# Optimization experiments

Measured on AMD Instinct MI355X. Metric: run time of the kernel, lower is better.

Reference implementation:

```python
import jax, jax.numpy as jnp
from jax import lax
import numpy as np

NUM_TAGS = 128
B, S = 256, 512


def setup_inputs() -> dict:
    key = jax.random.key(0)
    k1, k2, k3 = jax.random.split(key, 3)
    emissions = jax.random.normal(k1, (B, S, NUM_TAGS), dtype=jnp.float32)
    tags = jax.random.randint(k2, (B, S), 0, NUM_TAGS, dtype=jnp.int64)
    mask = jnp.ones((B, S), dtype=bool)
    transitions = jax.random.normal(k3, (NUM_TAGS, NUM_TAGS), dtype=jnp.float32)
    return {"emissions": emissions, "tags": tags, "mask": mask, "transitions": transitions}


def reference(emissions, tags, mask, transitions):
    # emissions: [B,S,C], tags: [B,S] int, mask: [B,S] bool, transitions: [C,C]
    m = mask.astype(emissions.dtype)

    # --- gold score (vectorized over time) ---
    emit = jnp.take_along_axis(emissions, tags[..., None], axis=2)[..., 0]  # [B,S]
    trans = transitions[tags[:, :-1], tags[:, 1:]]                           # [B,S-1]
    gold = jnp.sum(emit * m) + jnp.sum(trans * m[:, 1:])

    # --- partition via forward algorithm (note: original masks cancel out:
    # alpha*mask + alpha*~mask == alpha, so partition ignores mask) ---
    def step(alpha, e_t):
        # alpha: [B,C] prev log-alpha, e_t: [B,C] emissions at t
        score = alpha[:, :, None] + transitions[None, :, :] + e_t[:, None, :]  # [B,C,C]
        return jax.nn.logsumexp(score, axis=1), None

    alpha0 = emissions[:, 0]                       # [B,C]
    em_rest = jnp.swapaxes(emissions[:, 1:], 0, 1) # [S-1,B,C]
    alpha, _ = lax.scan(step, alpha0, em_rest)
    partition = jnp.sum(jax.nn.logsumexp(alpha, axis=1))

    # forward returns -log_likelihood = partition - gold
    return partition - gold
```

## Files before the change

### kernel.cpp

```cpp
#include <hip/hip_runtime.h>

#define NT 128
#define SS 512
#define PW 132

typedef float f32x2 __attribute__((ext_vector_type(2)));

__device__ __forceinline__ float rdlane(float v, int lane) {
    return __int_as_float(__builtin_amdgcn_readlane(__float_as_int(v), lane));
}
__device__ __forceinline__ int fexp_of(float x) {
    return (int)((__float_as_uint(x) >> 23) & 0xFFu) - 127;
}
__device__ __forceinline__ void lds_barrier() {
    asm volatile("s_waitcnt lgkmcnt(0)\n\ts_barrier" ::: "memory");
}

__global__ void zero_out_kernel(float* out) { out[0] = 0.0f; }

__global__ __launch_bounds__(256, 1) void crf_fwd_kernel(
    const float* __restrict__ emissions,
    const int* __restrict__ tags,
    const unsigned char* __restrict__ mask,
    const float* __restrict__ trans,
    float* __restrict__ out)
{
    const int b   = blockIdx.x;
    const int tid = threadIdx.x;
    const int l   = tid & 63;
    const int w   = tid >> 6;
    const int st  = (w << 5) + (l & 31);

    __shared__ float pbuf[2][4 * PW];
    __shared__ int   kbuf[4];
    __shared__ float redf[4];
    __shared__ float redg[4];

    const float*         emB = emissions + (size_t)b * SS * NT;
    const int*           tgB = tags + b * SS;
    const unsigned char* mkB = mask + b * SS;

    float gold = 0.0f;
    for (int t = tid; t < SS; t += 256) {
        int tg   = tgB[t];
        float mk = mkB[t] ? 1.0f : 0.0f;
        float a  = emB[(size_t)t * NT + tg];
        if (t > 0) a += trans[tgB[t - 1] * NT + tg];
        gold += a * mk;
    }

    f32x2 eTr[32];
    #pragma unroll
    for (int r = 0; r < 32; r++) {
        const float* row = trans + (size_t)((w << 5) + r) * NT;
        f32x2 v; v.x = __expf(row[l]); v.y = __expf(row[l + 64]);
        eTr[r] = v;
    }

    float a0 = emB[st];
    {
        float v = a0;
        #pragma unroll
        for (int o = 16; o > 0; o >>= 1) v = fmaxf(v, __shfl_xor(v, o));
        if (l == 0) redf[w] = v;
    }
    __syncthreads();
    const float M0 = fmaxf(fmaxf(redf[0], redf[1]), fmaxf(redf[2], redf[3]));

    float p = __expf(a0 - M0);
    float S = 0.0f;
    int K = 0, kv_own = 0;

    float ex_o = __expf(emB[(size_t)1 * NT + st]);
    float ex_e = __expf(emB[(size_t)2 * NT + st]);
    float pd_o = emB[(size_t)3 * NT + st];
    float pd_e = emB[(size_t)4 * NT + st];

    auto matvec = [&](int q, bool kw) -> float {
        f32x2 A0 = {0.f,0.f}, A1 = {0.f,0.f}, A2 = {0.f,0.f}, A3 = {0.f,0.f};
        #pragma unroll
        for (int r = 0; r < 32; r += 4) {
            float q0 = rdlane(p, r + 0);
            float q1 = rdlane(p, r + 1);
            float q2 = rdlane(p, r + 2);
            float q3 = rdlane(p, r + 3);
            f32x2 b0 = {q0, q0}, b1 = {q1, q1}, b2 = {q2, q2}, b3 = {q3, q3};
            A0 = __builtin_elementwise_fma(b0, eTr[r + 0], A0);
            A1 = __builtin_elementwise_fma(b1, eTr[r + 1], A1);
            A2 = __builtin_elementwise_fma(b2, eTr[r + 2], A2);
            A3 = __builtin_elementwise_fma(b3, eTr[r + 3], A3);
        }
        f32x2 s2 = (A0 + A1) + (A2 + A3);
        pbuf[q][w * PW + l]      = s2.x;
        pbuf[q][w * PW + l + 64] = s2.y;
        if (kw && l == 0) kbuf[w] = kv_own;
        lds_barrier();
        return (pbuf[q][0 * PW + st] + pbuf[q][1 * PW + st]) +
               (pbuf[q][2 * PW + st] + pbuf[q][3 * PW + st]);
    };
    auto rot = [&](int t, float& pd, float& ex) {
        float nr = pd;
        int tn = t + 4; if (tn > SS - 1) tn = SS - 1;
        pd = emB[(size_t)tn * NT + st];
        ex = __expf(nr);
    };

    #pragma unroll 1
    for (int t = 1; t < SS; t += 4) {
        {
            float sn = matvec(1, false) * ex_o;
            p = ldexpf(sn, -K);
            S += (float)K;
            int kv = fexp_of(p);
            #pragma unroll
            for (int o = 16; o > 0; o >>= 1) kv = max(kv, __shfl_xor(kv, o));
            kv_own = kv;
            rot(t, pd_o, ex_o);
        }
        if (t + 1 < SS) {
            float sn = matvec(0, true) * ex_e;
            int k0 = kbuf[0], k1 = kbuf[1], k2 = kbuf[2], k3 = kbuf[3];
            K = max(max(k0, k1), max(k2, k3));
            p = sn;
            rot(t + 1, pd_e, ex_e);
        }
        if (t + 2 < SS) { p = matvec(1, false) * ex_o; rot(t + 2, pd_o, ex_o); }
        if (t + 3 < SS) { p = matvec(0, false) * ex_e; rot(t + 3, pd_e, ex_e); }
    }

    {
        float sw = (l < 32) ? p : 0.0f;
        float g  = gold;
        #pragma unroll
        for (int o = 32; o > 0; o >>= 1) {
            sw += __shfl_xor(sw, o);
            g  += __shfl_xor(g, o);
        }
        if (l == 0) { redf[w] = sw; redg[w] = g; }
    }
    __syncthreads();
    if (tid == 0) {
        float tot  = (redf[0] + redf[1]) + (redf[2] + redf[3]);
        float part = M0 + S * 0.69314718055994531f + __logf(tot);
        float gt   = (redg[0] + redg[1]) + (redg[2] + redg[3]);
        atomicAdd(out, part - gt);
    }
}

extern "C" void kernel_launch(void* const* d_in, const int* in_sizes, int n_in,
                              void* d_out, int out_size, void* d_ws, size_t ws_size,
                              hipStream_t stream) {
    const float*         emissions = (const float*)d_in[0];
    const int*           tags      = (const int*)d_in[1];
    const unsigned char* mask      = (const unsigned char*)d_in[2];
    const float*         trans     = (const float*)d_in[3];
    float*               out       = (float*)d_out;

    zero_out_kernel<<<1, 1, 0, stream>>>(out);
    crf_fwd_kernel<<<256, 256, 0, stream>>>(emissions, tags, mask, trans, out);
}
```

Before: 240.8 us.

## Split CRF forward step across two waves with SGPR-operand packed FMAs

```diff
diff --git a/kernel.cpp b/kernel.cpp
--- a/kernel.cpp
+++ b/kernel.cpp
@@ -2,12 +2,11 @@
 
 #define NT 128
 #define SS 512
-#define PW 132
 
 typedef float f32x2 __attribute__((ext_vector_type(2)));
 
-__device__ __forceinline__ float rdlane(float v, int lane) {
-    return __int_as_float(__builtin_amdgcn_readlane(__float_as_int(v), lane));
+__device__ __forceinline__ int rdlane_i(float v, int lane) {
+    return __builtin_amdgcn_readlane(__float_as_int(v), lane);
 }
 __device__ __forceinline__ int fexp_of(float x) {
     return (int)((__float_as_uint(x) >> 23) & 0xFFu) - 127;
@@ -15,10 +14,17 @@
 __device__ __forceinline__ void lds_barrier() {
     asm volatile("s_waitcnt lgkmcnt(0)\n\ts_barrier" ::: "memory");
 }
+__device__ __forceinline__ void pkfma_s(f32x2& acc, unsigned long long qq, f32x2 etr) {
+    asm("v_pk_fma_f32 %0, %1, %2, %0" : "+v"(acc) : "s"(qq), "v"(etr));
+}
+__device__ __forceinline__ unsigned long long dup2(int q) {
+    unsigned u = (unsigned)q;
+    return ((unsigned long long)u << 32) | u;
+}
 
 __global__ void zero_out_kernel(float* out) { out[0] = 0.0f; }
 
-__global__ __launch_bounds__(256, 1) void crf_fwd_kernel(
+__global__ __launch_bounds__(128, 1) void crf_fwd_kernel(
     const float* __restrict__ emissions,
     const int* __restrict__ tags,
     const unsigned char* __restrict__ mask,
@@ -29,19 +35,22 @@
     const int tid = threadIdx.x;
     const int l   = tid & 63;
     const int w   = tid >> 6;
-    const int st  = (w << 5) + (l & 31);
+    const int st  = (w << 6) + l;
+    const int co  = ((w ^ 1) << 6) + l;
 
-    __shared__ float pbuf[2][4 * PW];
-    __shared__ int   kbuf[4];
-    __shared__ float redf[4];
-    __shared__ float redg[4];
+    __shared__ float pb[2][2][64];
+    __shared__ int   kslot;
+    __shared__ float redf[2];
+    __shared__ float redg[2];
 
     const float*         emB = emissions + (size_t)b * SS * NT;
     const int*           tgB = tags + b * SS;
     const unsigned char* mkB = mask + b * SS;
 
     float gold = 0.0f;
-    for (int t = tid; t < SS; t += 256) {
+    #pragma unroll
+    for (int k = 0; k < SS / 128; k++) {
+        int t    = tid + 128 * k;
         int tg   = tgB[t];
         float mk = mkB[t] ? 1.0f : 0.0f;
         float a  = emB[(size_t)t * NT + tg];
@@ -49,11 +58,11 @@
         gold += a * mk;
     }
 
-    f32x2 eTr[32];
+    f32x2 eTr[64];
     #pragma unroll
-    for (int r = 0; r < 32; r++) {
-        const float* row = trans + (size_t)((w << 5) + r) * NT;
-        f32x2 v; v.x = __expf(row[l]); v.y = __expf(row[l + 64]);
+    for (int r = 0; r < 64; r++) {
+        const float* row = trans + (size_t)((w << 6) + r) * NT;
+        f32x2 v; v.x = __expf(row[st]); v.y = __expf(row[co]);
         eTr[r] = v;
     }
 
@@ -61,11 +70,11 @@
     {
         float v = a0;
         #pragma unroll
-        for (int o = 16; o > 0; o >>= 1) v = fmaxf(v, __shfl_xor(v, o));
+        for (int o = 32; o > 0; o >>= 1) v = fmaxf(v, __shfl_xor(v, o));
         if (l == 0) redf[w] = v;
     }
     __syncthreads();
-    const float M0 = fmaxf(fmaxf(redf[0], redf[1]), fmaxf(redf[2], redf[3]));
+    const float M0 = fmaxf(redf[0], redf[1]);
 
     float p = __expf(a0 - M0);
     float S = 0.0f;
@@ -76,27 +85,20 @@
     float pd_o = emB[(size_t)3 * NT + st];
     float pd_e = emB[(size_t)4 * NT + st];
 
-    auto matvec = [&](int q, bool kw) -> float {
+    auto matvec = [&]() -> f32x2 {
         f32x2 A0 = {0.f,0.f}, A1 = {0.f,0.f}, A2 = {0.f,0.f}, A3 = {0.f,0.f};
         #pragma unroll
-        for (int r = 0; r < 32; r += 4) {
-            float q0 = rdlane(p, r + 0);
-            float q1 = rdlane(p, r + 1);
-            float q2 = rdlane(p, r + 2);
-            float q3 = rdlane(p, r + 3);
-            f32x2 b0 = {q0, q0}, b1 = {q1, q1}, b2 = {q2, q2}, b3 = {q3, q3};
-            A0 = __builtin_elementwise_fma(b0, eTr[r + 0], A0);
-            A1 = __builtin_elementwise_fma(b1, eTr[r + 1], A1);
-            A2 = __builtin_elementwise_fma(b2, eTr[r + 2], A2);
-            A3 = __builtin_elementwise_fma(b3, eTr[r + 3], A3);
+        for (int r = 0; r < 64; r += 4) {
+            unsigned long long q0 = dup2(rdlane_i(p, r + 0));
+            unsigned long long q1 = dup2(rdlane_i(p, r + 1));
+            unsigned long long q2 = dup2(rdlane_i(p, r + 2));
+            unsigned long long q3 = dup2(rdlane_i(p, r + 3));
+            pkfma_s(A0, q0, eTr[r + 0]);
+            pkfma_s(A1, q1, eTr[r + 1]);
+            pkfma_s(A2, q2, eTr[r + 2]);
+            pkfma_s(A3, q3, eTr[r + 3]);
         }
-        f32x2 s2 = (A0 + A1) + (A2 + A3);
-        pbuf[q][w * PW + l]      = s2.x;
-        pbuf[q][w * PW + l + 64] = s2.y;
-        if (kw && l == 0) kbuf[w] = kv_own;
-        lds_barrier();
-        return (pbuf[q][0 * PW + st] + pbuf[q][1 * PW + st]) +
-               (pbuf[q][2 * PW + st] + pbuf[q][3 * PW + st]);
+        return (A0 + A1) + (A2 + A3);
     };
     auto rot = [&](int t, float& pd, float& ex) {
         float nr = pd;
@@ -108,28 +110,42 @@
     #pragma unroll 1
     for (int t = 1; t < SS; t += 4) {
         {
-            float sn = matvec(1, false) * ex_o;
+            f32x2 s2 = matvec();
+            pb[w][1][l] = s2.y;
+            lds_barrier();
+            float sn = (s2.x + pb[w ^ 1][1][l]) * ex_o;
             p = ldexpf(sn, -K);
             S += (float)K;
-            int kv = fexp_of(p);
-            #pragma unroll
-            for (int o = 16; o > 0; o >>= 1) kv = max(kv, __shfl_xor(kv, o));
-            kv_own = kv;
+            kv_own = fexp_of(p);
             rot(t, pd_o, ex_o);
         }
         if (t + 1 < SS) {
-            float sn = matvec(0, true) * ex_e;
-            int k0 = kbuf[0], k1 = kbuf[1], k2 = kbuf[2], k3 = kbuf[3];
-            K = max(max(k0, k1), max(k2, k3));
-            p = sn;
+            f32x2 s2 = matvec();
+            pb[w][0][l] = s2.y;
+            if (w == 0 && l == 0) kslot = kv_own;
+            lds_barrier();
+            p = (s2.x + pb[w ^ 1][0][l]) * ex_e;
+            K = kslot;
             rot(t + 1, pd_e, ex_e);
         }
-        if (t + 2 < SS) { p = matvec(1, false) * ex_o; rot(t + 2, pd_o, ex_o); }
-        if (t + 3 < SS) { p = matvec(0, false) * ex_e; rot(t + 3, pd_e, ex_e); }
+        if (t + 2 < SS) {
+            f32x2 s2 = matvec();
+            pb[w][1][l] = s2.y;
+            lds_barrier();
+            p = (s2.x + pb[w ^ 1][1][l]) * ex_o;
+            rot(t + 2, pd_o, ex_o);
+        }
+        if (t + 3 < SS) {
+            f32x2 s2 = matvec();
+            pb[w][0][l] = s2.y;
+            lds_barrier();
+            p = (s2.x + pb[w ^ 1][0][l]) * ex_e;
+            rot(t + 3, pd_e, ex_e);
+        }
     }
 
     {
-        float sw = (l < 32) ? p : 0.0f;
+        float sw = p;
         float g  = gold;
         #pragma unroll
         for (int o = 32; o > 0; o >>= 1) {
@@ -140,9 +156,9 @@
     }
     __syncthreads();
     if (tid == 0) {
-        float tot  = (redf[0] + redf[1]) + (redf[2] + redf[3]);
+        float tot  = redf[0] + redf[1];
         float part = M0 + S * 0.69314718055994531f + __logf(tot);
-        float gt   = (redg[0] + redg[1]) + (redg[2] + redg[3]);
+        float gt   = redg[0] + redg[1];
         atomicAdd(out, part - gt);
     }
 }
@@ -157,5 +173,5 @@
     float*               out       = (float*)d_out;
 
     zero_out_kernel<<<1, 1, 0, stream>>>(out);
-    crf_fwd_kernel<<<256, 256, 0, stream>>>(emissions, tags, mask, trans, out);
+    crf_fwd_kernel<<<256, 128, 0, stream>>>(emissions, tags, mask, trans, out);
 }
```

Result: slower. 408.1 us (+69.5%).

## Process two batch rows per block to share barriers and interleave recurrences

Applied to the files above, without the earlier changes.

```diff
diff --git a/kernel.cpp b/kernel.cpp
--- a/kernel.cpp
+++ b/kernel.cpp
@@ -6,7 +6,7 @@
 
 typedef float f32x2 __attribute__((ext_vector_type(2)));
 
-__device__ __forceinline__ float rdlane(float v, int lane) {
+__device__ __forceinline__ float rdlanef(float v, int lane) {
     return __int_as_float(__builtin_amdgcn_readlane(__float_as_int(v), lane));
 }
 __device__ __forceinline__ int fexp_of(float x) {
@@ -25,28 +25,37 @@
     const float* __restrict__ trans,
     float* __restrict__ out)
 {
-    const int b   = blockIdx.x;
     const int tid = threadIdx.x;
     const int l   = tid & 63;
     const int w   = tid >> 6;
     const int st  = (w << 5) + (l & 31);
-
-    __shared__ float pbuf[2][4 * PW];
-    __shared__ int   kbuf[4];
-    __shared__ float redf[4];
-    __shared__ float redg[4];
-
-    const float*         emB = emissions + (size_t)b * SS * NT;
-    const int*           tgB = tags + b * SS;
-    const unsigned char* mkB = mask + b * SS;
-
-    float gold = 0.0f;
+    const int bA  = blockIdx.x * 2;
+    const int bB  = bA + 1;
+
+    __shared__ float pbuf[2][2][4 * PW];
+    __shared__ int   kslotA, kslotB;
+    __shared__ float redf[2][4];
+    __shared__ float redg[2][4];
+
+    const float*         emA  = emissions + (size_t)bA * SS * NT;
+    const float*         emBs = emissions + (size_t)bB * SS * NT;
+    const int*           tgA  = tags + bA * SS;
+    const int*           tgB  = tags + bB * SS;
+    const unsigned char* mkA  = mask + bA * SS;
+    const unsigned char* mkB  = mask + bB * SS;
+
+    float goldA = 0.0f, goldB = 0.0f;
     for (int t = tid; t < SS; t += 256) {
-        int tg   = tgB[t];
-        float mk = mkB[t] ? 1.0f : 0.0f;
-        float a  = emB[(size_t)t * NT + tg];
-        if (t > 0) a += trans[tgB[t - 1] * NT + tg];
-        gold += a * mk;
+        int ta = tgA[t];
+        float ma = mkA[t] ? 1.0f : 0.0f;
+        float aa = emA[(size_t)t * NT + ta];
+        if (t > 0) aa += trans[tgA[t - 1] * NT + ta];
+        goldA += aa * ma;
+        int tb = tgB[t];
+        float mb = mkB[t] ? 1.0f : 0.0f;
+        float ab = emBs[(size_t)t * NT + tb];
+        if (t > 0) ab += trans[tgB[t - 1] * NT + tb];
+        goldB += ab * mb;
     }
 
     f32x2 eTr[32];
@@ -57,93 +66,133 @@
         eTr[r] = v;
     }
 
-    float a0 = emB[st];
+    float a0A = emA[st], a0B = emBs[st];
     {
-        float v = a0;
+        float vA = a0A, vB = a0B;
         #pragma unroll
-        for (int o = 16; o > 0; o >>= 1) v = fmaxf(v, __shfl_xor(v, o));
-        if (l == 0) redf[w] = v;
+        for (int o = 16; o > 0; o >>= 1) {
+            vA = fmaxf(vA, __shfl_xor(vA, o));
+            vB = fmaxf(vB, __shfl_xor(vB, o));
+        }
+        if (l == 0) { redf[0][w] = vA; redf[1][w] = vB; }
     }
     __syncthreads();
-    const float M0 = fmaxf(fmaxf(redf[0], redf[1]), fmaxf(redf[2], redf[3]));
-
-    float p = __expf(a0 - M0);
-    float S = 0.0f;
-    int K = 0, kv_own = 0;
-
-    float ex_o = __expf(emB[(size_t)1 * NT + st]);
-    float ex_e = __expf(emB[(size_t)2 * NT + st]);
-    float pd_o = emB[(size_t)3 * NT + st];
-    float pd_e = emB[(size_t)4 * NT + st];
-
-    auto matvec = [&](int q, bool kw) -> float {
+    const float M0A = fmaxf(fmaxf(redf[0][0], redf[0][1]), fmaxf(redf[0][2], redf[0][3]));
+    const float M0B = fmaxf(fmaxf(redf[1][0], redf[1][1]), fmaxf(redf[1][2], redf[1][3]));
+
+    float pA = __expf(a0A - M0A);
+    float pB = __expf(a0B - M0B);
+    float SA = 0.0f, SB = 0.0f;
+    int KA = 0, KB = 0, kvA = 0, kvB = 0;
+
+    float exA_o = __expf(emA[(size_t)1 * NT + st]);
+    float exA_e = __expf(emA[(size_t)2 * NT + st]);
+    float pdA_o = emA[(size_t)3 * NT + st];
+    float pdA_e = emA[(size_t)4 * NT + st];
+    float exB_o = __expf(emBs[(size_t)1 * NT + st]);
+    float exB_e = __expf(emBs[(size_t)2 * NT + st]);
+    float pdB_o = emBs[(size_t)3 * NT + st];
+    float pdB_e = emBs[(size_t)4 * NT + st];
+
+    auto matvec = [&](float pp) -> f32x2 {
         f32x2 A0 = {0.f,0.f}, A1 = {0.f,0.f}, A2 = {0.f,0.f}, A3 = {0.f,0.f};
         #pragma unroll
         for (int r = 0; r < 32; r += 4) {
-            float q0 = rdlane(p, r + 0);
-            float q1 = rdlane(p, r + 1);
-            float q2 = rdlane(p, r + 2);
-            float q3 = rdlane(p, r + 3);
+            float q0 = rdlanef(pp, r + 0);
+            float q1 = rdlanef(pp, r + 1);
+            float q2 = rdlanef(pp, r + 2);
+            float q3 = rdlanef(pp, r + 3);
             f32x2 b0 = {q0, q0}, b1 = {q1, q1}, b2 = {q2, q2}, b3 = {q3, q3};
             A0 = __builtin_elementwise_fma(b0, eTr[r + 0], A0);
             A1 = __builtin_elementwise_fma(b1, eTr[r + 1], A1);
             A2 = __builtin_elementwise_fma(b2, eTr[r + 2], A2);
             A3 = __builtin_elementwise_fma(b3, eTr[r + 3], A3);
         }
-        f32x2 s2 = (A0 + A1) + (A2 + A3);
-        pbuf[q][w * PW + l]      = s2.x;
-        pbuf[q][w * PW + l + 64] = s2.y;
-        if (kw && l == 0) kbuf[w] = kv_own;
-        lds_barrier();
-        return (pbuf[q][0 * PW + st] + pbuf[q][1 * PW + st]) +
-               (pbuf[q][2 * PW + st] + pbuf[q][3 * PW + st]);
-    };
-    auto rot = [&](int t, float& pd, float& ex) {
+        return (A0 + A1) + (A2 + A3);
+    };
+    auto comb = [&](int q, int s) -> float {
+        return (pbuf[q][s][0 * PW + st] + pbuf[q][s][1 * PW + st]) +
+               (pbuf[q][s][2 * PW + st] + pbuf[q][s][3 * PW + st]);
+    };
+    auto wr = [&](int q, int s, f32x2 v) {
+        pbuf[q][s][w * PW + l]      = v.x;
+        pbuf[q][s][w * PW + l + 64] = v.y;
+    };
+    auto rot = [&](const float* em, int t, float& pd, float& ex) {
         float nr = pd;
         int tn = t + 4; if (tn > SS - 1) tn = SS - 1;
-        pd = emB[(size_t)tn * NT + st];
+        pd = em[(size_t)tn * NT + st];
         ex = __expf(nr);
     };
 
     #pragma unroll 1
     for (int t = 1; t < SS; t += 4) {
         {
-            float sn = matvec(1, false) * ex_o;
-            p = ldexpf(sn, -K);
-            S += (float)K;
-            int kv = fexp_of(p);
-            #pragma unroll
-            for (int o = 16; o > 0; o >>= 1) kv = max(kv, __shfl_xor(kv, o));
-            kv_own = kv;
-            rot(t, pd_o, ex_o);
+            f32x2 sA = matvec(pA); f32x2 sB = matvec(pB);
+            wr(1, 0, sA); wr(1, 1, sB);
+            lds_barrier();
+            float cA = comb(1, 0), cB = comb(1, 1);
+            pA = ldexpf(cA * exA_o, -KA); SA += (float)KA;
+            pB = ldexpf(cB * exB_o, -KB); SB += (float)KB;
+            kvA = fexp_of(pA);
+            kvB = fexp_of(pB);
+            rot(emA, t, pdA_o, exA_o);
+            rot(emBs, t, pdB_o, exB_o);
         }
         if (t + 1 < SS) {
-            float sn = matvec(0, true) * ex_e;
-            int k0 = kbuf[0], k1 = kbuf[1], k2 = kbuf[2], k3 = kbuf[3];
-            K = max(max(k0, k1), max(k2, k3));
-            p = sn;
-            rot(t + 1, pd_e, ex_e);
-        }
-        if (t + 2 < SS) { p = matvec(1, false) * ex_o; rot(t + 2, pd_o, ex_o); }
-        if (t + 3 < SS) { p = matvec(0, false) * ex_e; rot(t + 3, pd_e, ex_e); }
+            f32x2 sA = matvec(pA); f32x2 sB = matvec(pB);
+            wr(0, 0, sA); wr(0, 1, sB);
+            if (w == 0 && l == 0) { kslotA = kvA; kslotB = kvB; }
+            lds_barrier();
+            pA = comb(0, 0) * exA_e;
+            pB = comb(0, 1) * exB_e;
+            KA = kslotA; KB = kslotB;
+            rot(emA, t + 1, pdA_e, exA_e);
+            rot(emBs, t + 1, pdB_e, exB_e);
+        }
+        if (t + 2 < SS) {
+            f32x2 sA = matvec(pA); f32x2 sB = matvec(pB);
+            wr(1, 0, sA); wr(1, 1, sB);
+            lds_barrier();
+            pA = comb(1, 0) * exA_o;
+            pB = comb(1, 1) * exB_o;
+            rot(emA, t + 2, pdA_o, exA_o);
+            rot(emBs, t + 2, pdB_o, exB_o);
+        }
+        if (t + 3 < SS) {
+            f32x2 sA = matvec(pA); f32x2 sB = matvec(pB);
+            wr(0, 0, sA); wr(0, 1, sB);
+            lds_barrier();
+            pA = comb(0, 0) * exA_e;
+            pB = comb(0, 1) * exB_e;
+            rot(emA, t + 3, pdA_e, exA_e);
+            rot(emBs, t + 3, pdB_e, exB_e);
+        }
     }
 
     {
-        float sw = (l < 32) ? p : 0.0f;
-        float g  = gold;
+        float swA = (l < 32) ? pA : 0.0f;
+        float swB = (l < 32) ? pB : 0.0f;
+        float gA = goldA, gB = goldB;
         #pragma unroll
         for (int o = 32; o > 0; o >>= 1) {
-            sw += __shfl_xor(sw, o);
-            g  += __shfl_xor(g, o);
-        }
-        if (l == 0) { redf[w] = sw; redg[w] = g; }
+            swA += __shfl_xor(swA, o);
+            swB += __shfl_xor(swB, o);
+            gA  += __shfl_xor(gA, o);
+            gB  += __shfl_xor(gB, o);
+        }
+        if (l == 0) { redf[0][w] = swA; redf[1][w] = swB;
+                      redg[0][w] = gA;  redg[1][w] = gB; }
     }
     __syncthreads();
     if (tid == 0) {
-        float tot  = (redf[0] + redf[1]) + (redf[2] + redf[3]);
-        float part = M0 + S * 0.69314718055994531f + __logf(tot);
-        float gt   = (redg[0] + redg[1]) + (redg[2] + redg[3]);
-        atomicAdd(out, part - gt);
+        float totA = (redf[0][0] + redf[0][1]) + (redf[0][2] + redf[0][3]);
+        float totB = (redf[1][0] + redf[1][1]) + (redf[1][2] + redf[1][3]);
+        float gtA  = (redg[0][0] + redg[0][1]) + (redg[0][2] + redg[0][3]);
+        float gtB  = (redg[1][0] + redg[1][1]) + (redg[1][2] + redg[1][3]);
+        float partA = M0A + SA * 0.69314718055994531f + __logf(totA);
+        float partB = M0B + SB * 0.69314718055994531f + __logf(totB);
+        atomicAdd(out, (partA - gtA) + (partB - gtB));
     }
 }
 
@@ -157,5 +206,5 @@
     float*               out       = (float*)d_out;
 
     zero_out_kernel<<<1, 1, 0, stream>>>(out);
-    crf_fwd_kernel<<<256, 256, 0, stream>>>(emissions, tags, mask, trans, out);
-}
+    crf_fwd_kernel<<<128, 256, 0, stream>>>(emissions, tags, mask, trans, out);
+}
```

Result: slower. 348.2 us (+44.6%).
